# Kernel tuning notes

Hardware: AMD Instinct MI355X
Metric: run time of the kernel (lower is better)

The kernel has to match this reference:

```python
import jax, jax.numpy as jnp
import numpy as np

E, H = 512, 256  # embed_dim, hidden_dim
B, SQ, SK = 2, 512, 512


def _linear_params(k, fin, fout):
    lim = 1.0 / np.sqrt(fin)
    kw, kb = jax.random.split(k)
    W = jax.random.uniform(kw, (fin, fout), minval=-lim, maxval=lim, dtype=jnp.float32)
    b = jax.random.uniform(kb, (fout,), minval=-lim, maxval=lim, dtype=jnp.float32)
    return W, b


def setup_inputs() -> dict:
    rng = jax.random.key(0)
    ks = jax.random.split(rng, 12)
    query = jax.random.normal(ks[0], (B, SQ, E), dtype=jnp.float32)
    key = jax.random.normal(ks[1], (B, SK, E), dtype=jnp.float32)
    Wqe, bqe = _linear_params(ks[2], E, H)
    Wke, bke = _linear_params(ks[3], E, H)
    W1, b1 = _linear_params(ks[4], 2 * H, H)  # importance_predictor layer 0
    W2, b2 = _linear_params(ks[5], H, H)      # layer 1
    W3, b3 = _linear_params(ks[6], H, H)      # layer 2
    Wf, bf = _linear_params(ks[7], H, 1)      # final importance logit
    Wv1, bv1 = _linear_params(ks[8], 2 * H, H)  # variance_estimator layer 0
    Wv2, bv2 = _linear_params(ks[9], H, 1)      # variance_estimator final
    return {"query": query, "key": key,
            "Wqe": Wqe, "bqe": bqe, "Wke": Wke, "bke": bke,
            "W1": W1, "b1": b1, "W2": W2, "b2": b2, "W3": W3, "b3": b3,
            "Wf": Wf, "bf": bf, "Wv1": Wv1, "bv1": bv1, "Wv2": Wv2, "bv2": bv2}


def reference(query, key, Wqe, bqe, Wke, bke, W1, b1, W2, b2, W3, b3, Wf, bf, Wv1, bv1, Wv2, bv2):
    # Encoders (dropout is identity at eval)
    qf = jax.nn.relu(jnp.einsum('bqe,eh->bqh', query, Wqe) + bqe)  # [B,Sq,H]
    kf = jax.nn.relu(jnp.einsum('bke,eh->bkh', key, Wke) + bke)    # [B,Sk,H]

    # First Linear(2H,H) on cat([q,k]) == q@W1[:H] + k@W1[H:]; broadcast over pairs
    qp = jnp.einsum('bqh,hd->bqd', qf, W1[:H])
    kp = jnp.einsum('bkh,hd->bkd', kf, W1[H:])
    h = jax.nn.relu(qp[:, :, None, :] + kp[:, None, :, :] + b1)  # [B,Sq,Sk,H]
    h = jax.nn.relu(jnp.einsum('bqkh,hd->bqkd', h, W2) + b2)
    h = jax.nn.relu(jnp.einsum('bqkh,hd->bqkd', h, W3) + b3)
    importance_logits = (jnp.einsum('bqkh,ho->bqko', h, Wf) + bf)[..., 0]  # [B,Sq,Sk]

    # Variance head: Linear(2H,H) split the same way, ReLU, Linear, Softplus
    vq = jnp.einsum('bqh,hd->bqd', qf, Wv1[:H])
    vk = jnp.einsum('bkh,hd->bkd', kf, Wv1[H:])
    v = jax.nn.relu(vq[:, :, None, :] + vk[:, None, :, :] + bv1)  # [B,Sq,Sk,H]
    estimated_variance = jax.nn.softplus((jnp.einsum('bqkh,ho->bqko', v, Wv2) + bv2)[..., 0])
    return importance_logits, estimated_variance
```

## Files before the change

kernel.cpp:

```cpp
#include <hip/hip_runtime.h>
#include <hip/hip_bf16.h>
#include <cstdint>
#include <cstddef>
#include <cstring>

#define HDIM 256
#define EDIM 512
#define NB   2
#define NSQ  512
#define NSK  512

typedef _Float16 f16x8 __attribute__((ext_vector_type(8)));
typedef _Float16 h2    __attribute__((ext_vector_type(2)));
typedef __fp16   fp16v2 __attribute__((ext_vector_type(2)));
typedef float    f32x4  __attribute__((ext_vector_type(4)));

#define OFF_W2F  0u
#define OFF_W3F  65536u
#define OFF_WQEF 131072u
#define OFF_WKEF 262144u
#define OFF_WCQ  393216u
#define OFF_WCK  524288u
#define OFF_WV2H 655360u
#define F16_WS_END_BYTES 1312768u

union U8 { f16x8 v; h2 h[4]; };

__device__ __forceinline__ ushort2 f2h2(float x, float y) {
  fp16v2 r = __builtin_amdgcn_cvt_pkrtz(x, y);
  ushort2 u;
  __builtin_memcpy(&u, &r, 4);
  return u;
}
__device__ __forceinline__ float relu_(float x) { return x > 0.f ? x : 0.f; }
__device__ __forceinline__ float softplus_(float x) {
  return fmaxf(x, 0.f) + log1pf(expf(-fabsf(x)));
}

__global__ __launch_bounds__(256) void shuffle_weights(
    const float* __restrict__ Wqe, const float* __restrict__ Wke,
    const float* __restrict__ W1,  const float* __restrict__ Wv1,
    const float* __restrict__ W2,  const float* __restrict__ W3,
    const float* __restrict__ Wv2,
    unsigned short* __restrict__ wsb)
{
  __shared__ float sW[32 * 257];
  const int bx = blockIdx.x;
  const int t = threadIdx.x;
  if (bx == 80) {
    if (t < 64) {
      float a = Wv2[t * 4 + 0], b = Wv2[t * 4 + 1];
      float c = Wv2[t * 4 + 2], d = Wv2[t * 4 + 3];
      ushort2 lo = f2h2(a, b), hi = f2h2(c, d);
      ushort4 o; o.x = lo.x; o.y = lo.y; o.z = hi.x; o.w = hi.y;
      *(ushort4*)&wsb[OFF_WV2H + t * 4] = o;
    }
    return;
  }
  const float* src; unsigned short* dst; int s; int S;
  if      (bx <  8) { src = W2;          dst = wsb + OFF_W2F;           s = bx;      S = 8;  }
  else if (bx < 16) { src = W3;          dst = wsb + OFF_W3F;           s = bx - 8;  S = 8;  }
  else if (bx < 32) { src = Wqe;         dst = wsb + OFF_WQEF;          s = bx - 16; S = 16; }
  else if (bx < 48) { src = Wke;         dst = wsb + OFF_WKEF;          s = bx - 32; S = 16; }
  else if (bx < 56) { src = W1;          dst = wsb + OFF_WCQ;           s = bx - 48; S = 8;  }
  else if (bx < 64) { src = Wv1;         dst = wsb + OFF_WCQ + 65536u;  s = bx - 56; S = 8;  }
  else if (bx < 72) { src = W1 + 65536;  dst = wsb + OFF_WCK;           s = bx - 64; S = 8;  }
  else              { src = Wv1 + 65536; dst = wsb + OFF_WCK + 65536u;  s = bx - 72; S = 8;  }

  const int kbase = s * 32;
  #pragma unroll
  for (int it = 0; it < 8; ++it) {
    const int f4 = it * 256 + t;
    const int row = f4 >> 6, c4 = (f4 & 63) * 4;
    float4 v = *(const float4*)(src + (size_t)(kbase + row) * 256 + c4);
    sW[row * 257 + c4 + 0] = v.x; sW[row * 257 + c4 + 1] = v.y;
    sW[row * 257 + c4 + 2] = v.z; sW[row * 257 + c4 + 3] = v.w;
  }
  __syncthreads();

  const int wave = t >> 6, lane = t & 63;
  const int n_in = lane & 15, k0 = (lane >> 4) * 8;
  for (int tt = wave * 4; tt < wave * 4 + 4; ++tt) {
    const int n = tt * 16 + n_in;
    float x[8];
    #pragma unroll
    for (int j = 0; j < 8; ++j) x[j] = sW[(k0 + j) * 257 + n];
    ushort2 p0 = f2h2(x[0], x[1]), p1 = f2h2(x[2], x[3]);
    ushort2 p2 = f2h2(x[4], x[5]), p3 = f2h2(x[6], x[7]);
    ushort4 lo; lo.x = p0.x; lo.y = p0.y; lo.z = p1.x; lo.w = p1.y;
    ushort4 hi; hi.x = p2.x; hi.y = p2.y; hi.z = p3.x; hi.w = p3.y;
    unsigned short* o = dst + ((size_t)(tt * S + s) * 64 + lane) * 8;
    *(ushort4*)&o[0] = lo; *(ushort4*)&o[4] = hi;
  }
}

__global__ __launch_bounds__(512) void encoder_kernel(
    const float* __restrict__ query, const float* __restrict__ key,
    const float* __restrict__ bqe,   const float* __restrict__ bke,
    const float* __restrict__ b1,    const float* __restrict__ bv1,
    const unsigned short* __restrict__ WqeF, const unsigned short* __restrict__ WkeF,
    const unsigned short* __restrict__ WcqF, const unsigned short* __restrict__ WckF,
    _Float16* __restrict__ Pq, _Float16* __restrict__ Pk)
{
  __shared__ unsigned short sX[16 * 520];
  __shared__ unsigned short sF[16 * 264];
  __shared__ float sBe[256];
  __shared__ float sBc[512];

  const int bx   = blockIdx.x;
  const int side = bx >> 8;
  const int idx  = bx & 255;
  const int rt   = idx >> 2;
  const int nh   = idx & 3;
  const int t    = threadIdx.x;

  const float* Xsrc = side ? key : query;
  const unsigned short* WeF = side ? WkeF : WqeF;
  const unsigned short* WcF = side ? WckF : WcqF;
  _Float16* P = side ? Pk : Pq;

  const int wave = t >> 6, lane = t & 63;
  const int l15 = lane & 15, q4 = lane >> 4;

  const unsigned short* aeb = WeF + ((size_t)(wave * 2) * 16 * 64 + lane) * 8;
  f16x8 afe[2][2];
  #pragma unroll
  for (int ft = 0; ft < 2; ++ft)
    afe[0][ft] = *(const f16x8*)(aeb + ft * 8192);

  {
    const int m = t >> 5, ch = t & 31;
    const float* xr = Xsrc + (size_t)(rt * 16 + m) * EDIM;
    #pragma unroll
    for (int j = 0; j < 4; ++j) {
      const int c = j * 128 + ch * 4;
      float4 v = *(const float4*)(xr + c);
      ushort2 lo = f2h2(v.x, v.y), hi = f2h2(v.z, v.w);
      ushort4 xb; xb.x = lo.x; xb.y = lo.y; xb.z = hi.x; xb.w = hi.y;
      *(ushort4*)&sX[m * 520 + c] = xb;
    }
    if (t < 256) {
      sBe[t]       = side ? bke[t] : bqe[t];
      sBc[t]       = side ? 0.f : b1[t];
      sBc[256 + t] = side ? 0.f : bv1[t];
    }
  }
  __syncthreads();

  f32x4 acc1[2];
  #pragma unroll
  for (int ft = 0; ft < 2; ++ft) acc1[ft] = (f32x4){0.f, 0.f, 0.f, 0.f};

  #pragma unroll
  for (int s = 0; s < 16; ++s) {
    if (s < 15) {
      #pragma unroll
      for (int ft = 0; ft < 2; ++ft)
        afe[(s + 1) & 1][ft] = *(const f16x8*)(aeb + ft * 8192 + (size_t)(s + 1) * 512);
    }
    f16x8 bfr = *(const f16x8*)&sX[l15 * 520 + s * 32 + q4 * 8];
    #pragma unroll
    for (int ft = 0; ft < 2; ++ft)
      acc1[ft] = __builtin_amdgcn_mfma_f32_16x16x32_f16(afe[s & 1][ft], bfr, acc1[ft], 0, 0, 0);
  }

  #pragma unroll
  for (int ft = 0; ft < 2; ++ft) {
    const int tg = wave * 2 + ft;
    const int n0 = tg * 16 + q4 * 4;
    float4 b4 = *(const float4*)&sBe[n0];
    f32x4 a = acc1[ft];
    ushort2 lo = f2h2(relu_(a[0] + b4.x), relu_(a[1] + b4.y));
    ushort2 hi = f2h2(relu_(a[2] + b4.z), relu_(a[3] + b4.w));
    ushort4 h; h.x = lo.x; h.y = lo.y; h.z = hi.x; h.w = hi.y;
    *(ushort4*)&sF[l15 * 264 + n0] = h;
  }
  __syncthreads();

  const int tg2 = nh * 8 + wave;
  const unsigned short* acb = WcF + ((size_t)tg2 * 8 * 64 + lane) * 8;
  f16x8 afc[2];
  afc[0] = *(const f16x8*)(acb);

  f32x4 acc2 = (f32x4){0.f, 0.f, 0.f, 0.f};

  #pragma unroll
  for (int s = 0; s < 8; ++s) {
    if (s < 7)
      afc[(s + 1) & 1] = *(const f16x8*)(acb + (size_t)(s + 1) * 512);
    f16x8 bfr = *(const f16x8*)&sF[l15 * 264 + s * 32 + q4 * 8];
    acc2 = __builtin_amdgcn_mfma_f32_16x16x32_f16(afc[s & 1], bfr, acc2, 0, 0, 0);
  }

  {
    const int n0 = tg2 * 16 + q4 * 4;
    float4 bc = *(const float4*)&sBc[n0];
    const int row = rt * 16 + l15;
    ushort2 lo = f2h2(acc2[0] + bc.x, acc2[1] + bc.y);
    ushort2 hi = f2h2(acc2[2] + bc.z, acc2[3] + bc.w);
    ushort4 o; o.x = lo.x; o.y = lo.y; o.z = hi.x; o.w = hi.y;
    *(ushort4*)((unsigned short*)P + (size_t)row * 512 + n0) = o;
  }
}

__global__ __launch_bounds__(512, 4) void pair_kernel(
    const _Float16* __restrict__ Pq, const _Float16* __restrict__ Pk,
    const unsigned short* __restrict__ W2F, const unsigned short* __restrict__ W3F,
    const float* __restrict__ b2, const float* __restrict__ b3,
    const float* __restrict__ Wf, const float* __restrict__ bfp,
    const unsigned short* __restrict__ Wv2H, const float* __restrict__ bv2p,
    float* __restrict__ out)
{
  __shared__ __align__(16) unsigned char smem[69632];
  unsigned short* sXH = (unsigned short*)smem;
  unsigned short* sH  = (unsigned short*)(smem + 33792);
  float* sRed = (float*)(smem + 67584);

  const int kt = blockIdx.x, qy = blockIdx.y, bz = blockIdx.z;
  const int t = threadIdx.x;
  const _Float16* qpRow = Pq + (size_t)(bz * NSQ + qy) * 512;

  const int wave = t >> 6, lane = t & 63;
  const int l15 = lane & 15, q4 = lane >> 4;

  const unsigned short* a2base = W2F + ((size_t)(wave * 2) * 8 * 64 + lane) * 8;
  const unsigned short* a3base = W3F + ((size_t)(wave * 2) * 8 * 64 + lane) * 8;

  f16x8 afd[2][2];
  afd[0][0] = *(const f16x8*)(a2base);
  afd[0][1] = *(const f16x8*)(a2base + 8 * 64 * 8);

  float vp0 = 0.f, vp1 = 0.f;
  {
    const int m   = t >> 3;
    const int sub = t & 7;
    const _Float16* kpRow = Pk + (size_t)(bz * NSK + kt * 64 + m) * 512;
    const f16x8 z8 = {0, 0, 0, 0, 0, 0, 0, 0};
    #pragma unroll
    for (int it = 0; it < 4; ++it) {
      const int c = it * 64 + sub * 8;
      f16x8 q8 = *(const f16x8*)(qpRow + c);
      f16x8 k8 = *(const f16x8*)(kpRow + c);
      f16x8 r  = __builtin_elementwise_max(q8 + k8, z8);
      *(f16x8*)&sXH[m * 264 + c] = r;
      f16x8 a8 = *(const f16x8*)(qpRow + 256 + c);
      f16x8 v8 = *(const f16x8*)(kpRow + 256 + c);
      U8 ar; ar.v = __builtin_elementwise_max(a8 + v8, z8);
      U8 w8; w8.v = *(const f16x8*)((const _Float16*)Wv2H + c);
      vp0 = __builtin_amdgcn_fdot2(ar.h[0], w8.h[0], vp0, false);
      vp1 = __builtin_amdgcn_fdot2(ar.h[1], w8.h[1], vp1, false);
      vp0 = __builtin_amdgcn_fdot2(ar.h[2], w8.h[2], vp0, false);
      vp1 = __builtin_amdgcn_fdot2(ar.h[3], w8.h[3], vp1, false);
    }
  }
  __syncthreads();

  f32x4 acc[2][4];
  #pragma unroll
  for (int ft = 0; ft < 2; ++ft)
    #pragma unroll
    for (int pt = 0; pt < 4; ++pt)
      acc[ft][pt] = (f32x4){0.f, 0.f, 0.f, 0.f};

  f16x8 bcur[4], bnxt[4];
  #pragma unroll
  for (int pt = 0; pt < 4; ++pt)
    bcur[pt] = *(const f16x8*)&sXH[(pt * 16 + l15) * 264 + q4 * 8];

  #pragma unroll
  for (int s = 0; s < 8; ++s) {
    if (s < 7) {
      afd[(s + 1) & 1][0] = *(const f16x8*)(a2base + (size_t)(s + 1) * 512);
      afd[(s + 1) & 1][1] = *(const f16x8*)(a2base + 8 * 64 * 8 + (size_t)(s + 1) * 512);
      #pragma unroll
      for (int pt = 0; pt < 4; ++pt)
        bnxt[pt] = *(const f16x8*)&sXH[(pt * 16 + l15) * 264 + (s + 1) * 32 + q4 * 8];
    }
    __builtin_amdgcn_s_setprio(1);
    #pragma unroll
    for (int ft = 0; ft < 2; ++ft)
      #pragma unroll
      for (int pt = 0; pt < 4; ++pt)
        acc[ft][pt] = __builtin_amdgcn_mfma_f32_16x16x32_f16(afd[s & 1][ft], bcur[pt], acc[ft][pt], 0, 0, 0);
    __builtin_amdgcn_s_setprio(0);
    #pragma unroll
    for (int pt = 0; pt < 4; ++pt) bcur[pt] = bnxt[pt];
  }

  afd[0][0] = *(const f16x8*)(a3base);
  afd[0][1] = *(const f16x8*)(a3base + 8 * 64 * 8);

  #pragma unroll
  for (int ft = 0; ft < 2; ++ft) {
    const int tg = wave * 2 + ft;
    const int n0 = tg * 16 + q4 * 4;
    float4 b4 = *(const float4*)&b2[n0];
    #pragma unroll
    for (int pt = 0; pt < 4; ++pt) {
      const int mr = pt * 16 + l15;
      f32x4 a = acc[ft][pt];
      ushort2 lo = f2h2(relu_(a[0] + b4.x), relu_(a[1] + b4.y));
      ushort2 hi = f2h2(relu_(a[2] + b4.z), relu_(a[3] + b4.w));
      ushort4 h; h.x = lo.x; h.y = lo.y; h.z = hi.x; h.w = hi.y;
      *(ushort4*)&sH[mr * 264 + n0] = h;
    }
  }
  __syncthreads();

  f32x4 acc2[2][4];
  #pragma unroll
  for (int ft = 0; ft < 2; ++ft)
    #pragma unroll
    for (int pt = 0; pt < 4; ++pt)
      acc2[ft][pt] = (f32x4){0.f, 0.f, 0.f, 0.f};

  #pragma unroll
  for (int pt = 0; pt < 4; ++pt)
    bcur[pt] = *(const f16x8*)&sH[(pt * 16 + l15) * 264 + q4 * 8];

  #pragma unroll
  for (int s = 0; s < 8; ++s) {
    if (s < 7) {
      afd[(s + 1) & 1][0] = *(const f16x8*)(a3base + (size_t)(s + 1) * 512);
      afd[(s + 1) & 1][1] = *(const f16x8*)(a3base + 8 * 64 * 8 + (size_t)(s + 1) * 512);
      #pragma unroll
      for (int pt = 0; pt < 4; ++pt)
        bnxt[pt] = *(const f16x8*)&sH[(pt * 16 + l15) * 264 + (s + 1) * 32 + q4 * 8];
    }
    __builtin_amdgcn_s_setprio(1);
    #pragma unroll
    for (int ft = 0; ft < 2; ++ft)
      #pragma unroll
      for (int pt = 0; pt < 4; ++pt)
        acc2[ft][pt] = __builtin_amdgcn_mfma_f32_16x16x32_f16(afd[s & 1][ft], bcur[pt], acc2[ft][pt], 0, 0, 0);
    __builtin_amdgcn_s_setprio(0);
    #pragma unroll
    for (int pt = 0; pt < 4; ++pt) bcur[pt] = bnxt[pt];
  }

  {
    float v = vp0 + vp1;
    v += __shfl_xor(v, 1, 64);
    v += __shfl_xor(v, 2, 64);
    v += __shfl_xor(v, 4, 64);
    if ((t & 7) == 0) {
      const int m = t >> 3;
      const size_t o = (size_t)(bz * NSQ + qy) * NSK + kt * 64 + m;
      out[(size_t)NB * NSQ * NSK + o] = softplus_(v + bv2p[0]);
    }
  }

  float p[4] = {0.f, 0.f, 0.f, 0.f};
  #pragma unroll
  for (int ft = 0; ft < 2; ++ft) {
    const int tg = wave * 2 + ft;
    const int n0 = tg * 16 + q4 * 4;
    float4 b4 = *(const float4*)&b3[n0];
    float4 w4 = *(const float4*)&Wf[n0];
    #pragma unroll
    for (int pt = 0; pt < 4; ++pt) {
      f32x4 a = acc2[ft][pt];
      p[pt] += relu_(a[0] + b4.x) * w4.x + relu_(a[1] + b4.y) * w4.y
             + relu_(a[2] + b4.z) * w4.z + relu_(a[3] + b4.w) * w4.w;
    }
  }
  #pragma unroll
  for (int pt = 0; pt < 4; ++pt) {
    float v = p[pt];
    v += __shfl_xor(v, 16, 64);
    v += __shfl_xor(v, 32, 64);
    if (lane < 16) sRed[wave * 64 + pt * 16 + lane] = v;
  }
  __syncthreads();

  if (t < 64) {
    const size_t o = (size_t)(bz * NSQ + qy) * NSK + kt * 64 + t;
    float lg = bfp[0];
    #pragma unroll
    for (int w = 0; w < 8; ++w) lg += sRed[w * 64 + t];
    out[o] = lg;
  }
}

extern "C" void kernel_launch(void* const* d_in, const int* in_sizes, int n_in,
                              void* d_out, int out_size, void* d_ws, size_t ws_size,
                              hipStream_t stream)
{
  (void)in_sizes; (void)n_in; (void)out_size; (void)ws_size;
  const float* query = (const float*)d_in[0];
  const float* key   = (const float*)d_in[1];
  const float* Wqe   = (const float*)d_in[2];
  const float* bqe   = (const float*)d_in[3];
  const float* Wke   = (const float*)d_in[4];
  const float* bke   = (const float*)d_in[5];
  const float* W1    = (const float*)d_in[6];
  const float* b1    = (const float*)d_in[7];
  const float* W2    = (const float*)d_in[8];
  const float* b2    = (const float*)d_in[9];
  const float* W3    = (const float*)d_in[10];
  const float* b3    = (const float*)d_in[11];
  const float* Wf    = (const float*)d_in[12];
  const float* bf    = (const float*)d_in[13];
  const float* Wv1   = (const float*)d_in[14];
  const float* bv1   = (const float*)d_in[15];
  const float* Wv2   = (const float*)d_in[16];
  const float* bv2   = (const float*)d_in[17];

  unsigned short* wsb = (unsigned short*)d_ws;
  _Float16* Pq = (_Float16*)((char*)d_ws + F16_WS_END_BYTES);
  _Float16* Pk = Pq + (size_t)1024 * 512;
  float* out = (float*)d_out;

  shuffle_weights<<<81, 256, 0, stream>>>(Wqe, Wke, W1, Wv1, W2, W3, Wv2, wsb);
  encoder_kernel<<<512, 512, 0, stream>>>(query, key, bqe, bke, b1, bv1,
      wsb + OFF_WQEF, wsb + OFF_WKEF, wsb + OFF_WCQ, wsb + OFF_WCK, Pq, Pk);
  pair_kernel<<<dim3(NSK / 64, NSQ, NB), 512, 0, stream>>>(Pq, Pk,
      wsb + OFF_W2F, wsb + OFF_W3F, b2, b3, Wf, bf, wsb + OFF_WV2H, bv2, out);
}
```

Measured before the change: 255.1 us.

## Make pair kernel persistent over key tiles with async LDS staging of key projections

Each block now handles one query row and loops over all eight 64-key tiles, instead of launching one block per (key tile, query) pair. Raw key projections are staged into LDS with global_load_lds, and the next tile is prefetched while the second GEMM runs. The q+k add and ReLU are fused into the MFMA operand load. This cuts the block count and the per-block setup and repeated loads, but gives eight times fewer blocks and adds a serial loop with extra barriers per tile.

```diff
diff --git a/kernel.cpp b/kernel.cpp
--- a/kernel.cpp
+++ b/kernel.cpp
@@ -211,175 +211,227 @@
     const unsigned short* __restrict__ Wv2H, const float* __restrict__ bv2p,
     float* __restrict__ out)
 {
-  __shared__ __align__(16) unsigned char smem[69632];
-  unsigned short* sXH = (unsigned short*)smem;
+  __shared__ __align__(16) unsigned char smem[70656];
+  unsigned short* sKP = (unsigned short*)smem;
   unsigned short* sH  = (unsigned short*)(smem + 33792);
-  float* sRed = (float*)(smem + 67584);
-
-  const int kt = blockIdx.x, qy = blockIdx.y, bz = blockIdx.z;
+  unsigned short* sQP = (unsigned short*)(smem + 67584);
+  float* sRed = (float*)(smem + 68608);
+
+  const int qy = blockIdx.x, bz = blockIdx.y;
   const int t = threadIdx.x;
-  const _Float16* qpRow = Pq + (size_t)(bz * NSQ + qy) * 512;
 
   const int wave = t >> 6, lane = t & 63;
   const int l15 = lane & 15, q4 = lane >> 4;
+  const int m8 = t >> 3, sub = t & 7;
+
+  const _Float16* qpRow = Pq + (size_t)(bz * NSQ + qy) * 512;
+  const _Float16* PkB   = Pk + (size_t)(bz * NSK) * 512;
 
   const unsigned short* a2base = W2F + ((size_t)(wave * 2) * 8 * 64 + lane) * 8;
   const unsigned short* a3base = W3F + ((size_t)(wave * 2) * 8 * 64 + lane) * 8;
 
+  const f16x8 z8 = {0, 0, 0, 0, 0, 0, 0, 0};
+
+  #define STAGE_KP(ktile)                                                      \
+    do {                                                                       \
+      const _Float16* kb_ = PkB + (size_t)(ktile) * 64 * 512;                  \
+      _Pragma("unroll")                                                        \
+      for (int i_ = 0; i_ < 4; ++i_) {                                         \
+        const int chunk_ = i_ * 512 + t;                                       \
+        const int r_ = chunk_ / 33;                                            \
+        const int c_ = chunk_ - r_ * 33;                                       \
+        const int cc_ = (c_ == 32) ? 0 : c_;                                   \
+        const _Float16* g_ = kb_ + (size_t)r_ * 512 + cc_ * 8;                 \
+        unsigned short* l_ = sKP + (size_t)(i_ * 512 + (t & ~63)) * 8;         \
+        __builtin_amdgcn_global_load_lds(                                      \
+            (const __attribute__((address_space(1))) unsigned int*)g_,         \
+            (__attribute__((address_space(3))) unsigned int*)l_, 16, 0, 0);    \
+      }                                                                        \
+      if (t < 64) {                                                            \
+        const int chunk_ = 2048 + t;                                           \
+        const int r_ = chunk_ / 33;                                            \
+        const int c_ = chunk_ - r_ * 33;                                       \
+        const int cc_ = (c_ == 32) ? 0 : c_;                                   \
+        const _Float16* g_ = kb_ + (size_t)r_ * 512 + cc_ * 8;                 \
+        unsigned short* l_ = sKP + (size_t)2048 * 8;                           \
+        __builtin_amdgcn_global_load_lds(                                      \
+            (const __attribute__((address_space(1))) unsigned int*)g_,         \
+            (__attribute__((address_space(3))) unsigned int*)l_, 16, 0, 0);    \
+      }                                                                        \
+    } while (0)
+
+  if (t < 64) *(f16x8*)&sQP[t * 8] = *(const f16x8*)(qpRow + t * 8);
+  STAGE_KP(0);
   f16x8 afd[2][2];
   afd[0][0] = *(const f16x8*)(a2base);
-  afd[0][1] = *(const f16x8*)(a2base + 8 * 64 * 8);
-
-  float vp0 = 0.f, vp1 = 0.f;
-  {
-    const int m   = t >> 3;
-    const int sub = t & 7;
-    const _Float16* kpRow = Pk + (size_t)(bz * NSK + kt * 64 + m) * 512;
-    const f16x8 z8 = {0, 0, 0, 0, 0, 0, 0, 0};
-    #pragma unroll
-    for (int it = 0; it < 4; ++it) {
-      const int c = it * 64 + sub * 8;
-      f16x8 q8 = *(const f16x8*)(qpRow + c);
-      f16x8 k8 = *(const f16x8*)(kpRow + c);
-      f16x8 r  = __builtin_elementwise_max(q8 + k8, z8);
-      *(f16x8*)&sXH[m * 264 + c] = r;
-      f16x8 a8 = *(const f16x8*)(qpRow + 256 + c);
-      f16x8 v8 = *(const f16x8*)(kpRow + 256 + c);
-      U8 ar; ar.v = __builtin_elementwise_max(a8 + v8, z8);
-      U8 w8; w8.v = *(const f16x8*)((const _Float16*)Wv2H + c);
-      vp0 = __builtin_amdgcn_fdot2(ar.h[0], w8.h[0], vp0, false);
-      vp1 = __builtin_amdgcn_fdot2(ar.h[1], w8.h[1], vp1, false);
-      vp0 = __builtin_amdgcn_fdot2(ar.h[2], w8.h[2], vp0, false);
-      vp1 = __builtin_amdgcn_fdot2(ar.h[3], w8.h[3], vp1, false);
-    }
-  }
+  afd[0][1] = *(const f16x8*)(a2base + 4096);
   __syncthreads();
 
-  f32x4 acc[2][4];
-  #pragma unroll
-  for (int ft = 0; ft < 2; ++ft)
+  for (int kt = 0; kt < 8; ++kt) {
+    f32x4 acc[2][4];
+    #pragma unroll
+    for (int ft = 0; ft < 2; ++ft)
+      #pragma unroll
+      for (int pt = 0; pt < 4; ++pt)
+        acc[ft][pt] = (f32x4){0.f, 0.f, 0.f, 0.f};
+
+    f16x8 bcur[4], brnx[4];
+    {
+      f16x8 qpf = *(const f16x8*)&sQP[q4 * 8];
+      #pragma unroll
+      for (int pt = 0; pt < 4; ++pt) {
+        f16x8 raw = *(const f16x8*)&sKP[(pt * 16 + l15) * 264 + q4 * 8];
+        bcur[pt] = __builtin_elementwise_max(raw + qpf, z8);
+      }
+    }
+
+    #pragma unroll
+    for (int s = 0; s < 8; ++s) {
+      f16x8 qpn;
+      if (s < 7) {
+        afd[(s + 1) & 1][0] = *(const f16x8*)(a2base + (size_t)(s + 1) * 512);
+        afd[(s + 1) & 1][1] = *(const f16x8*)(a2base + 4096 + (size_t)(s + 1) * 512);
+        qpn = *(const f16x8*)&sQP[(s + 1) * 32 + q4 * 8];
+        #pragma unroll
+        for (int pt = 0; pt < 4; ++pt)
+          brnx[pt] = *(const f16x8*)&sKP[(pt * 16 + l15) * 264 + (s + 1) * 32 + q4 * 8];
+      }
+      __builtin_amdgcn_s_setprio(1);
+      #pragma unroll
+      for (int ft = 0; ft < 2; ++ft)
+        #pragma unroll
+        for (int pt = 0; pt < 4; ++pt)
+          acc[ft][pt] = __builtin_amdgcn_mfma_f32_16x16x32_f16(afd[s & 1][ft], bcur[pt], acc[ft][pt], 0, 0, 0);
+      __builtin_amdgcn_s_setprio(0);
+      if (s < 7) {
+        #pragma unroll
+        for (int pt = 0; pt < 4; ++pt)
+          bcur[pt] = __builtin_elementwise_max(brnx[pt] + qpn, z8);
+      }
+    }
+
+    afd[0][0] = *(const f16x8*)(a3base);
+    afd[0][1] = *(const f16x8*)(a3base + 4096);
+
+    #pragma unroll
+    for (int ft = 0; ft < 2; ++ft) {
+      const int tg = wave * 2 + ft;
+      const int n0 = tg * 16 + q4 * 4;
+      float4 b4 = *(const float4*)&b2[n0];
+      #pragma unroll
+      for (int pt = 0; pt < 4; ++pt) {
+        const int mr = pt * 16 + l15;
+        f32x4 a = acc[ft][pt];
+        ushort2 lo = f2h2(relu_(a[0] + b4.x), relu_(a[1] + b4.y));
+        ushort2 hi = f2h2(relu_(a[2] + b4.z), relu_(a[3] + b4.w));
+        ushort4 h; h.x = lo.x; h.y = lo.y; h.z = hi.x; h.w = hi.y;
+        *(ushort4*)&sH[mr * 264 + n0] = h;
+      }
+    }
+    __syncthreads();
+
+    if (kt < 7) STAGE_KP(kt + 1);
+
+    f16x8 kv[4];
+    {
+      const _Float16* kvRow = PkB + ((size_t)(kt * 64 + m8)) * 512 + 256;
+      #pragma unroll
+      for (int it = 0; it < 4; ++it)
+        kv[it] = *(const f16x8*)(kvRow + it * 64 + sub * 8);
+    }
+
+    #pragma unroll
+    for (int ft = 0; ft < 2; ++ft)
+      #pragma unroll
+      for (int pt = 0; pt < 4; ++pt)
+        acc[ft][pt] = (f32x4){0.f, 0.f, 0.f, 0.f};
+
     #pragma unroll
     for (int pt = 0; pt < 4; ++pt)
-      acc[ft][pt] = (f32x4){0.f, 0.f, 0.f, 0.f};
-
-  f16x8 bcur[4], bnxt[4];
-  #pragma unroll
-  for (int pt = 0; pt < 4; ++pt)
-    bcur[pt] = *(const f16x8*)&sXH[(pt * 16 + l15) * 264 + q4 * 8];
-
-  #pragma unroll
-  for (int s = 0; s < 8; ++s) {
-    if (s < 7) {
-      afd[(s + 1) & 1][0] = *(const f16x8*)(a2base + (size_t)(s + 1) * 512);
-      afd[(s + 1) & 1][1] = *(const f16x8*)(a2base + 8 * 64 * 8 + (size_t)(s + 1) * 512);
-      #pragma unroll
-      for (int pt = 0; pt < 4; ++pt)
-        bnxt[pt] = *(const f16x8*)&sXH[(pt * 16 + l15) * 264 + (s + 1) * 32 + q4 * 8];
-    }
-    __builtin_amdgcn_s_setprio(1);
-    #pragma unroll
-    for (int ft = 0; ft < 2; ++ft)
-      #pragma unroll
-      for (int pt = 0; pt < 4; ++pt)
-        acc[ft][pt] = __builtin_amdgcn_mfma_f32_16x16x32_f16(afd[s & 1][ft], bcur[pt], acc[ft][pt], 0, 0, 0);
-    __builtin_amdgcn_s_setprio(0);
-    #pragma unroll
-    for (int pt = 0; pt < 4; ++pt) bcur[pt] = bnxt[pt];
-  }
-
-  afd[0][0] = *(const f16x8*)(a3base);
-  afd[0][1] = *(const f16x8*)(a3base + 8 * 64 * 8);
-
-  #pragma unroll
-  for (int ft = 0; ft < 2; ++ft) {
-    const int tg = wave * 2 + ft;
-    const int n0 = tg * 16 + q4 * 4;
-    float4 b4 = *(const float4*)&b2[n0];
-    #pragma unroll
-    for (int pt = 0; pt < 4; ++pt) {
-      const int mr = pt * 16 + l15;
-      f32x4 a = acc[ft][pt];
-      ushort2 lo = f2h2(relu_(a[0] + b4.x), relu_(a[1] + b4.y));
-      ushort2 hi = f2h2(relu_(a[2] + b4.z), relu_(a[3] + b4.w));
-      ushort4 h; h.x = lo.x; h.y = lo.y; h.z = hi.x; h.w = hi.y;
-      *(ushort4*)&sH[mr * 264 + n0] = h;
-    }
-  }
-  __syncthreads();
-
-  f32x4 acc2[2][4];
-  #pragma unroll
-  for (int ft = 0; ft < 2; ++ft)
-    #pragma unroll
-    for (int pt = 0; pt < 4; ++pt)
-      acc2[ft][pt] = (f32x4){0.f, 0.f, 0.f, 0.f};
-
-  #pragma unroll
-  for (int pt = 0; pt < 4; ++pt)
-    bcur[pt] = *(const f16x8*)&sH[(pt * 16 + l15) * 264 + q4 * 8];
-
-  #pragma unroll
-  for (int s = 0; s < 8; ++s) {
-    if (s < 7) {
-      afd[(s + 1) & 1][0] = *(const f16x8*)(a3base + (size_t)(s + 1) * 512);
-      afd[(s + 1) & 1][1] = *(const f16x8*)(a3base + 8 * 64 * 8 + (size_t)(s + 1) * 512);
-      #pragma unroll
-      for (int pt = 0; pt < 4; ++pt)
-        bnxt[pt] = *(const f16x8*)&sH[(pt * 16 + l15) * 264 + (s + 1) * 32 + q4 * 8];
-    }
-    __builtin_amdgcn_s_setprio(1);
-    #pragma unroll
-    for (int ft = 0; ft < 2; ++ft)
-      #pragma unroll
-      for (int pt = 0; pt < 4; ++pt)
-        acc2[ft][pt] = __builtin_amdgcn_mfma_f32_16x16x32_f16(afd[s & 1][ft], bcur[pt], acc2[ft][pt], 0, 0, 0);
-    __builtin_amdgcn_s_setprio(0);
-    #pragma unroll
-    for (int pt = 0; pt < 4; ++pt) bcur[pt] = bnxt[pt];
-  }
-
-  {
-    float v = vp0 + vp1;
-    v += __shfl_xor(v, 1, 64);
-    v += __shfl_xor(v, 2, 64);
-    v += __shfl_xor(v, 4, 64);
-    if ((t & 7) == 0) {
-      const int m = t >> 3;
-      const size_t o = (size_t)(bz * NSQ + qy) * NSK + kt * 64 + m;
-      out[(size_t)NB * NSQ * NSK + o] = softplus_(v + bv2p[0]);
-    }
-  }
-
-  float p[4] = {0.f, 0.f, 0.f, 0.f};
-  #pragma unroll
-  for (int ft = 0; ft < 2; ++ft) {
-    const int tg = wave * 2 + ft;
-    const int n0 = tg * 16 + q4 * 4;
-    float4 b4 = *(const float4*)&b3[n0];
-    float4 w4 = *(const float4*)&Wf[n0];
-    #pragma unroll
-    for (int pt = 0; pt < 4; ++pt) {
-      f32x4 a = acc2[ft][pt];
-      p[pt] += relu_(a[0] + b4.x) * w4.x + relu_(a[1] + b4.y) * w4.y
-             + relu_(a[2] + b4.z) * w4.z + relu_(a[3] + b4.w) * w4.w;
-    }
-  }
-  #pragma unroll
-  for (int pt = 0; pt < 4; ++pt) {
-    float v = p[pt];
-    v += __shfl_xor(v, 16, 64);
-    v += __shfl_xor(v, 32, 64);
-    if (lane < 16) sRed[wave * 64 + pt * 16 + lane] = v;
-  }
-  __syncthreads();
-
-  if (t < 64) {
-    const size_t o = (size_t)(bz * NSQ + qy) * NSK + kt * 64 + t;
-    float lg = bfp[0];
-    #pragma unroll
-    for (int w = 0; w < 8; ++w) lg += sRed[w * 64 + t];
-    out[o] = lg;
-  }
+      bcur[pt] = *(const f16x8*)&sH[(pt * 16 + l15) * 264 + q4 * 8];
+
+    #pragma unroll
+    for (int s = 0; s < 8; ++s) {
+      if (s < 7) {
+        afd[(s + 1) & 1][0] = *(const f16x8*)(a3base + (size_t)(s + 1) * 512);
+        afd[(s + 1) & 1][1] = *(const f16x8*)(a3base + 4096 + (size_t)(s + 1) * 512);
+        #pragma unroll
+        for (int pt = 0; pt < 4; ++pt)
+          brnx[pt] = *(const f16x8*)&sH[(pt * 16 + l15) * 264 + (s + 1) * 32 + q4 * 8];
+      }
+      __builtin_amdgcn_s_setprio(1);
+      #pragma unroll
+      for (int ft = 0; ft < 2; ++ft)
+        #pragma unroll
+        for (int pt = 0; pt < 4; ++pt)
+          acc[ft][pt] = __builtin_amdgcn_mfma_f32_16x16x32_f16(afd[s & 1][ft], bcur[pt], acc[ft][pt], 0, 0, 0);
+      __builtin_amdgcn_s_setprio(0);
+      if (s < 7) {
+        #pragma unroll
+        for (int pt = 0; pt < 4; ++pt) bcur[pt] = brnx[pt];
+      }
+    }
+
+    afd[0][0] = *(const f16x8*)(a2base);
+    afd[0][1] = *(const f16x8*)(a2base + 4096);
+
+    {
+      float vp0 = 0.f, vp1 = 0.f;
+      #pragma unroll
+      for (int it = 0; it < 4; ++it) {
+        const int c = it * 64 + sub * 8;
+        f16x8 qv8 = *(const f16x8*)&sQP[256 + c];
+        U8 ar; ar.v = __builtin_elementwise_max(kv[it] + qv8, z8);
+        U8 w8; w8.v = *(const f16x8*)((const _Float16*)Wv2H + c);
+        vp0 = __builtin_amdgcn_fdot2(ar.h[0], w8.h[0], vp0, false);
+        vp1 = __builtin_amdgcn_fdot2(ar.h[1], w8.h[1], vp1, false);
+        vp0 = __builtin_amdgcn_fdot2(ar.h[2], w8.h[2], vp0, false);
+        vp1 = __builtin_amdgcn_fdot2(ar.h[3], w8.h[3], vp1, false);
+      }
+      float v = vp0 + vp1;
+      v += __shfl_xor(v, 1, 64);
+      v += __shfl_xor(v, 2, 64);
+      v += __shfl_xor(v, 4, 64);
+      if (sub == 0) {
+        const size_t o = (size_t)(bz * NSQ + qy) * NSK + kt * 64 + m8;
+        out[(size_t)NB * NSQ * NSK + o] = softplus_(v + bv2p[0]);
+      }
+    }
+
+    {
+      float p[4] = {0.f, 0.f, 0.f, 0.f};
+      #pragma unroll
+      for (int ft = 0; ft < 2; ++ft) {
+        const int tg = wave * 2 + ft;
+        const int n0 = tg * 16 + q4 * 4;
+        float4 b4 = *(const float4*)&b3[n0];
+        float4 w4 = *(const float4*)&Wf[n0];
+        #pragma unroll
+        for (int pt = 0; pt < 4; ++pt) {
+          f32x4 a = acc[ft][pt];
+          p[pt] += relu_(a[0] + b4.x) * w4.x + relu_(a[1] + b4.y) * w4.y
+                 + relu_(a[2] + b4.z) * w4.z + relu_(a[3] + b4.w) * w4.w;
+        }
+      }
+      #pragma unroll
+      for (int pt = 0; pt < 4; ++pt) {
+        float v = p[pt];
+        v += __shfl_xor(v, 16, 64);
+        v += __shfl_xor(v, 32, 64);
+        if (lane < 16) sRed[wave * 64 + pt * 16 + lane] = v;
+      }
+    }
+    __syncthreads();
+
+    if (t < 64) {
+      const size_t o = (size_t)(bz * NSQ + qy) * NSK + kt * 64 + t;
+      float lg = bfp[0];
+      #pragma unroll
+      for (int w = 0; w < 8; ++w) lg += sRed[w * 64 + t];
+      out[o] = lg;
+    }
+  }
+  #undef STAGE_KP
 }
 
 extern "C" void kernel_launch(void* const* d_in, const int* in_sizes, int n_in,
@@ -414,6 +466,6 @@
   shuffle_weights<<<81, 256, 0, stream>>>(Wqe, Wke, W1, Wv1, W2, W3, Wv2, wsb);
   encoder_kernel<<<512, 512, 0, stream>>>(query, key, bqe, bke, b1, bv1,
       wsb + OFF_WQEF, wsb + OFF_WKEF, wsb + OFF_WCQ, wsb + OFF_WCK, Pq, Pk);
-  pair_kernel<<<dim3(NSK / 64, NSQ, NB), 512, 0, stream>>>(Pq, Pk,
+  pair_kernel<<<dim3(NSQ, NB), 512, 0, stream>>>(Pq, Pk,
       wsb + OFF_W2F, wsb + OFF_W3F, b2, b3, Wf, bf, wsb + OFF_WV2H, bv2, out);
 }
```

Result: slower. 537.0 us (+110.5%).

## Use 1024-thread pair blocks with one feature tile per wave and reuse LDS

Applied to the files above, without the earlier changes.

The pair kernel now runs 16 waves per block instead of 8. Each wave computes one 16-column feature tile instead of two, which halves per-wave accumulator registers. The second-layer hidden activations overwrite the input tile in shared memory, so shared memory per block roughly halves; this needs an extra barrier. Register double-buffering of the A and B fragments and the setprio hints are dropped, trading software prefetch for more resident waves to hide latency, and the final cross-wave reduction grows to 16 partials.

```diff
diff --git a/kernel.cpp b/kernel.cpp
--- a/kernel.cpp
+++ b/kernel.cpp
@@ -203,7 +203,7 @@
   }
 }
 
-__global__ __launch_bounds__(512, 4) void pair_kernel(
+__global__ __launch_bounds__(1024, 8) void pair_kernel(
     const _Float16* __restrict__ Pq, const _Float16* __restrict__ Pk,
     const unsigned short* __restrict__ W2F, const unsigned short* __restrict__ W3F,
     const float* __restrict__ b2, const float* __restrict__ b3,
@@ -211,34 +211,27 @@
     const unsigned short* __restrict__ Wv2H, const float* __restrict__ bv2p,
     float* __restrict__ out)
 {
-  __shared__ __align__(16) unsigned char smem[69632];
+  __shared__ __align__(16) unsigned char smem[37888];
   unsigned short* sXH = (unsigned short*)smem;
-  unsigned short* sH  = (unsigned short*)(smem + 33792);
-  float* sRed = (float*)(smem + 67584);
+  float* sRed = (float*)(smem + 33792);
 
   const int kt = blockIdx.x, qy = blockIdx.y, bz = blockIdx.z;
   const int t = threadIdx.x;
-  const _Float16* qpRow = Pq + (size_t)(bz * NSQ + qy) * 512;
 
   const int wave = t >> 6, lane = t & 63;
   const int l15 = lane & 15, q4 = lane >> 4;
 
-  const unsigned short* a2base = W2F + ((size_t)(wave * 2) * 8 * 64 + lane) * 8;
-  const unsigned short* a3base = W3F + ((size_t)(wave * 2) * 8 * 64 + lane) * 8;
-
-  f16x8 afd[2][2];
-  afd[0][0] = *(const f16x8*)(a2base);
-  afd[0][1] = *(const f16x8*)(a2base + 8 * 64 * 8);
+  const _Float16* qpRow = Pq + (size_t)(bz * NSQ + qy) * 512;
 
   float vp0 = 0.f, vp1 = 0.f;
   {
-    const int m   = t >> 3;
-    const int sub = t & 7;
+    const int m = t >> 4;
+    const int sub = t & 15;
     const _Float16* kpRow = Pk + (size_t)(bz * NSK + kt * 64 + m) * 512;
     const f16x8 z8 = {0, 0, 0, 0, 0, 0, 0, 0};
     #pragma unroll
-    for (int it = 0; it < 4; ++it) {
-      const int c = it * 64 + sub * 8;
+    for (int it = 0; it < 2; ++it) {
+      const int c = it * 128 + sub * 8;
       f16x8 q8 = *(const f16x8*)(qpRow + c);
       f16x8 k8 = *(const f16x8*)(kpRow + c);
       f16x8 r  = __builtin_elementwise_max(q8 + k8, z8);
@@ -255,87 +248,50 @@
   }
   __syncthreads();
 
-  f32x4 acc[2][4];
-  #pragma unroll
-  for (int ft = 0; ft < 2; ++ft)
-    #pragma unroll
-    for (int pt = 0; pt < 4; ++pt)
-      acc[ft][pt] = (f32x4){0.f, 0.f, 0.f, 0.f};
-
-  f16x8 bcur[4], bnxt[4];
-  #pragma unroll
-  for (int pt = 0; pt < 4; ++pt)
-    bcur[pt] = *(const f16x8*)&sXH[(pt * 16 + l15) * 264 + q4 * 8];
+  const unsigned short* a2 = W2F + (size_t)wave * 4096 + lane * 8;
+  const unsigned short* a3 = W3F + (size_t)wave * 4096 + lane * 8;
+  const int n0 = wave * 16 + q4 * 4;
+
+  f32x4 acc[4];
+  #pragma unroll
+  for (int pt = 0; pt < 4; ++pt) acc[pt] = (f32x4){0.f, 0.f, 0.f, 0.f};
 
   #pragma unroll
   for (int s = 0; s < 8; ++s) {
-    if (s < 7) {
-      afd[(s + 1) & 1][0] = *(const f16x8*)(a2base + (size_t)(s + 1) * 512);
-      afd[(s + 1) & 1][1] = *(const f16x8*)(a2base + 8 * 64 * 8 + (size_t)(s + 1) * 512);
-      #pragma unroll
-      for (int pt = 0; pt < 4; ++pt)
-        bnxt[pt] = *(const f16x8*)&sXH[(pt * 16 + l15) * 264 + (s + 1) * 32 + q4 * 8];
-    }
-    __builtin_amdgcn_s_setprio(1);
-    #pragma unroll
-    for (int ft = 0; ft < 2; ++ft)
-      #pragma unroll
-      for (int pt = 0; pt < 4; ++pt)
-        acc[ft][pt] = __builtin_amdgcn_mfma_f32_16x16x32_f16(afd[s & 1][ft], bcur[pt], acc[ft][pt], 0, 0, 0);
-    __builtin_amdgcn_s_setprio(0);
-    #pragma unroll
-    for (int pt = 0; pt < 4; ++pt) bcur[pt] = bnxt[pt];
-  }
-
-  afd[0][0] = *(const f16x8*)(a3base);
-  afd[0][1] = *(const f16x8*)(a3base + 8 * 64 * 8);
-
-  #pragma unroll
-  for (int ft = 0; ft < 2; ++ft) {
-    const int tg = wave * 2 + ft;
-    const int n0 = tg * 16 + q4 * 4;
+    f16x8 af = *(const f16x8*)(a2 + (size_t)s * 512);
+    #pragma unroll
+    for (int pt = 0; pt < 4; ++pt) {
+      f16x8 bf = *(const f16x8*)&sXH[(pt * 16 + l15) * 264 + s * 32 + q4 * 8];
+      acc[pt] = __builtin_amdgcn_mfma_f32_16x16x32_f16(af, bf, acc[pt], 0, 0, 0);
+    }
+  }
+  __syncthreads();
+
+  {
     float4 b4 = *(const float4*)&b2[n0];
     #pragma unroll
     for (int pt = 0; pt < 4; ++pt) {
       const int mr = pt * 16 + l15;
-      f32x4 a = acc[ft][pt];
+      f32x4 a = acc[pt];
       ushort2 lo = f2h2(relu_(a[0] + b4.x), relu_(a[1] + b4.y));
       ushort2 hi = f2h2(relu_(a[2] + b4.z), relu_(a[3] + b4.w));
       ushort4 h; h.x = lo.x; h.y = lo.y; h.z = hi.x; h.w = hi.y;
-      *(ushort4*)&sH[mr * 264 + n0] = h;
-    }
-  }
-  __syncthreads();
-
-  f32x4 acc2[2][4];
-  #pragma unroll
-  for (int ft = 0; ft < 2; ++ft)
-    #pragma unroll
-    for (int pt = 0; pt < 4; ++pt)
-      acc2[ft][pt] = (f32x4){0.f, 0.f, 0.f, 0.f};
-
-  #pragma unroll
-  for (int pt = 0; pt < 4; ++pt)
-    bcur[pt] = *(const f16x8*)&sH[(pt * 16 + l15) * 264 + q4 * 8];
+      *(ushort4*)&sXH[mr * 264 + n0] = h;
+    }
+  }
+  __syncthreads();
+
+  #pragma unroll
+  for (int pt = 0; pt < 4; ++pt) acc[pt] = (f32x4){0.f, 0.f, 0.f, 0.f};
 
   #pragma unroll
   for (int s = 0; s < 8; ++s) {
-    if (s < 7) {
-      afd[(s + 1) & 1][0] = *(const f16x8*)(a3base + (size_t)(s + 1) * 512);
-      afd[(s + 1) & 1][1] = *(const f16x8*)(a3base + 8 * 64 * 8 + (size_t)(s + 1) * 512);
-      #pragma unroll
-      for (int pt = 0; pt < 4; ++pt)
-        bnxt[pt] = *(const f16x8*)&sH[(pt * 16 + l15) * 264 + (s + 1) * 32 + q4 * 8];
-    }
-    __builtin_amdgcn_s_setprio(1);
-    #pragma unroll
-    for (int ft = 0; ft < 2; ++ft)
-      #pragma unroll
-      for (int pt = 0; pt < 4; ++pt)
-        acc2[ft][pt] = __builtin_amdgcn_mfma_f32_16x16x32_f16(afd[s & 1][ft], bcur[pt], acc2[ft][pt], 0, 0, 0);
-    __builtin_amdgcn_s_setprio(0);
-    #pragma unroll
-    for (int pt = 0; pt < 4; ++pt) bcur[pt] = bnxt[pt];
+    f16x8 af = *(const f16x8*)(a3 + (size_t)s * 512);
+    #pragma unroll
+    for (int pt = 0; pt < 4; ++pt) {
+      f16x8 bf = *(const f16x8*)&sXH[(pt * 16 + l15) * 264 + s * 32 + q4 * 8];
+      acc[pt] = __builtin_amdgcn_mfma_f32_16x16x32_f16(af, bf, acc[pt], 0, 0, 0);
+    }
   }
 
   {
@@ -343,33 +299,31 @@
     v += __shfl_xor(v, 1, 64);
     v += __shfl_xor(v, 2, 64);
     v += __shfl_xor(v, 4, 64);
-    if ((t & 7) == 0) {
-      const int m = t >> 3;
+    v += __shfl_xor(v, 8, 64);
+    if (l15 == 0) {
+      const int m = wave * 4 + q4;
       const size_t o = (size_t)(bz * NSQ + qy) * NSK + kt * 64 + m;
       out[(size_t)NB * NSQ * NSK + o] = softplus_(v + bv2p[0]);
     }
   }
 
-  float p[4] = {0.f, 0.f, 0.f, 0.f};
-  #pragma unroll
-  for (int ft = 0; ft < 2; ++ft) {
-    const int tg = wave * 2 + ft;
-    const int n0 = tg * 16 + q4 * 4;
+  {
+    float p[4] = {0.f, 0.f, 0.f, 0.f};
     float4 b4 = *(const float4*)&b3[n0];
     float4 w4 = *(const float4*)&Wf[n0];
     #pragma unroll
     for (int pt = 0; pt < 4; ++pt) {
-      f32x4 a = acc2[ft][pt];
+      f32x4 a = acc[pt];
       p[pt] += relu_(a[0] + b4.x) * w4.x + relu_(a[1] + b4.y) * w4.y
              + relu_(a[2] + b4.z) * w4.z + relu_(a[3] + b4.w) * w4.w;
     }
-  }
-  #pragma unroll
-  for (int pt = 0; pt < 4; ++pt) {
-    float v = p[pt];
-    v += __shfl_xor(v, 16, 64);
-    v += __shfl_xor(v, 32, 64);
-    if (lane < 16) sRed[wave * 64 + pt * 16 + lane] = v;
+    #pragma unroll
+    for (int pt = 0; pt < 4; ++pt) {
+      float v = p[pt];
+      v += __shfl_xor(v, 16, 64);
+      v += __shfl_xor(v, 32, 64);
+      if (lane < 16) sRed[wave * 64 + pt * 16 + lane] = v;
+    }
   }
   __syncthreads();
 
@@ -377,7 +331,7 @@
     const size_t o = (size_t)(bz * NSQ + qy) * NSK + kt * 64 + t;
     float lg = bfp[0];
     #pragma unroll
-    for (int w = 0; w < 8; ++w) lg += sRed[w * 64 + t];
+    for (int w = 0; w < 16; ++w) lg += sRed[w * 64 + t];
     out[o] = lg;
   }
 }
@@ -414,6 +368,6 @@
   shuffle_weights<<<81, 256, 0, stream>>>(Wqe, Wke, W1, Wv1, W2, W3, Wv2, wsb);
   encoder_kernel<<<512, 512, 0, stream>>>(query, key, bqe, bke, b1, bv1,
       wsb + OFF_WQEF, wsb + OFF_WKEF, wsb + OFF_WCQ, wsb + OFF_WCK, Pq, Pk);
-  pair_kernel<<<dim3(NSK / 64, NSQ, NB), 512, 0, stream>>>(Pq, Pk,
+  pair_kernel<<<dim3(NSK / 64, NSQ, NB), 1024, 0, stream>>>(Pq, Pk,
       wsb + OFF_W2F, wsb + OFF_W3F, b2, b3, Wf, bf, wsb + OFF_WV2H, bv2, out);
 }
```

Result: slower. 291.3 us (+14.2%).

## Retile pair-kernel MFMA work as 2x4 wave grid and drop register prefetch

Applied to the files above, without the earlier changes.

Each of the eight waves now owns a 32-row by 64-column output tile (2 M-groups by 4 N-groups) instead of 64 rows by 32 columns. Each wave therefore loads four global weight fragments and two LDS activation fragments per k-step, where before it loaded two and four. The cross-iteration double-buffered prefetch of A and B fragments is removed and fragments are loaded inside each step, which cuts register pressure. The reduction buffer shrinks to four partial rows. The trade-off is more global weight traffic per wave and less explicit latency hiding.

```diff
diff --git a/kernel.cpp b/kernel.cpp
--- a/kernel.cpp
+++ b/kernel.cpp
@@ -211,7 +211,7 @@
     const unsigned short* __restrict__ Wv2H, const float* __restrict__ bv2p,
     float* __restrict__ out)
 {
-  __shared__ __align__(16) unsigned char smem[69632];
+  __shared__ __align__(16) unsigned char smem[68608];
   unsigned short* sXH = (unsigned short*)smem;
   unsigned short* sH  = (unsigned short*)(smem + 33792);
   float* sRed = (float*)(smem + 67584);
@@ -222,13 +222,11 @@
 
   const int wave = t >> 6, lane = t & 63;
   const int l15 = lane & 15, q4 = lane >> 4;
-
-  const unsigned short* a2base = W2F + ((size_t)(wave * 2) * 8 * 64 + lane) * 8;
-  const unsigned short* a3base = W3F + ((size_t)(wave * 2) * 8 * 64 + lane) * 8;
-
-  f16x8 afd[2][2];
-  afd[0][0] = *(const f16x8*)(a2base);
-  afd[0][1] = *(const f16x8*)(a2base + 8 * 64 * 8);
+  const int mi = wave >> 2;
+  const int ni = wave & 3;
+
+  const unsigned short* a2base = W2F + ((size_t)(ni * 4) * 8 * 64 + lane) * 8;
+  const unsigned short* a3base = W3F + ((size_t)(ni * 4) * 8 * 64 + lane) * 8;
 
   float vp0 = 0.f, vp1 = 0.f;
   {
@@ -255,49 +253,39 @@
   }
   __syncthreads();
 
-  f32x4 acc[2][4];
-  #pragma unroll
-  for (int ft = 0; ft < 2; ++ft)
-    #pragma unroll
-    for (int pt = 0; pt < 4; ++pt)
+  f32x4 acc[4][2];
+  #pragma unroll
+  for (int ft = 0; ft < 4; ++ft)
+    #pragma unroll
+    for (int pt = 0; pt < 2; ++pt)
       acc[ft][pt] = (f32x4){0.f, 0.f, 0.f, 0.f};
 
-  f16x8 bcur[4], bnxt[4];
-  #pragma unroll
-  for (int pt = 0; pt < 4; ++pt)
-    bcur[pt] = *(const f16x8*)&sXH[(pt * 16 + l15) * 264 + q4 * 8];
-
   #pragma unroll
   for (int s = 0; s < 8; ++s) {
-    if (s < 7) {
-      afd[(s + 1) & 1][0] = *(const f16x8*)(a2base + (size_t)(s + 1) * 512);
-      afd[(s + 1) & 1][1] = *(const f16x8*)(a2base + 8 * 64 * 8 + (size_t)(s + 1) * 512);
+    f16x8 afd[4], bf[2];
+    #pragma unroll
+    for (int ft = 0; ft < 4; ++ft)
+      afd[ft] = *(const f16x8*)(a2base + ft * 4096 + (size_t)s * 512);
+    #pragma unroll
+    for (int pt = 0; pt < 2; ++pt)
+      bf[pt] = *(const f16x8*)&sXH[(mi * 32 + pt * 16 + l15) * 264 + s * 32 + q4 * 8];
+    __builtin_amdgcn_s_setprio(1);
+    #pragma unroll
+    for (int ft = 0; ft < 4; ++ft)
       #pragma unroll
-      for (int pt = 0; pt < 4; ++pt)
-        bnxt[pt] = *(const f16x8*)&sXH[(pt * 16 + l15) * 264 + (s + 1) * 32 + q4 * 8];
-    }
-    __builtin_amdgcn_s_setprio(1);
-    #pragma unroll
-    for (int ft = 0; ft < 2; ++ft)
-      #pragma unroll
-      for (int pt = 0; pt < 4; ++pt)
-        acc[ft][pt] = __builtin_amdgcn_mfma_f32_16x16x32_f16(afd[s & 1][ft], bcur[pt], acc[ft][pt], 0, 0, 0);
+      for (int pt = 0; pt < 2; ++pt)
+        acc[ft][pt] = __builtin_amdgcn_mfma_f32_16x16x32_f16(afd[ft], bf[pt], acc[ft][pt], 0, 0, 0);
     __builtin_amdgcn_s_setprio(0);
-    #pragma unroll
-    for (int pt = 0; pt < 4; ++pt) bcur[pt] = bnxt[pt];
-  }
-
-  afd[0][0] = *(const f16x8*)(a3base);
-  afd[0][1] = *(const f16x8*)(a3base + 8 * 64 * 8);
-
-  #pragma unroll
-  for (int ft = 0; ft < 2; ++ft) {
-    const int tg = wave * 2 + ft;
+  }
+
+  #pragma unroll
+  for (int ft = 0; ft < 4; ++ft) {
+    const int tg = ni * 4 + ft;
     const int n0 = tg * 16 + q4 * 4;
     float4 b4 = *(const float4*)&b2[n0];
     #pragma unroll
-    for (int pt = 0; pt < 4; ++pt) {
-      const int mr = pt * 16 + l15;
+    for (int pt = 0; pt < 2; ++pt) {
+      const int mr = mi * 32 + pt * 16 + l15;
       f32x4 a = acc[ft][pt];
       ushort2 lo = f2h2(relu_(a[0] + b4.x), relu_(a[1] + b4.y));
       ushort2 hi = f2h2(relu_(a[2] + b4.z), relu_(a[3] + b4.w));
@@ -307,35 +295,28 @@
   }
   __syncthreads();
 
-  f32x4 acc2[2][4];
-  #pragma unroll
-  for (int ft = 0; ft < 2; ++ft)
-    #pragma unroll
-    for (int pt = 0; pt < 4; ++pt)
-      acc2[ft][pt] = (f32x4){0.f, 0.f, 0.f, 0.f};
-
-  #pragma unroll
-  for (int pt = 0; pt < 4; ++pt)
-    bcur[pt] = *(const f16x8*)&sH[(pt * 16 + l15) * 264 + q4 * 8];
+  #pragma unroll
+  for (int ft = 0; ft < 4; ++ft)
+    #pragma unroll
+    for (int pt = 0; pt < 2; ++pt)
+      acc[ft][pt] = (f32x4){0.f, 0.f, 0.f, 0.f};
 
   #pragma unroll
   for (int s = 0; s < 8; ++s) {
-    if (s < 7) {
-      afd[(s + 1) & 1][0] = *(const f16x8*)(a3base + (size_t)(s + 1) * 512);
-      afd[(s + 1) & 1][1] = *(const f16x8*)(a3base + 8 * 64 * 8 + (size_t)(s + 1) * 512);
+    f16x8 afd[4], bf[2];
+    #pragma unroll
+    for (int ft = 0; ft < 4; ++ft)
+      afd[ft] = *(const f16x8*)(a3base + ft * 4096 + (size_t)s * 512);
+    #pragma unroll
+    for (int pt = 0; pt < 2; ++pt)
+      bf[pt] = *(const f16x8*)&sH[(mi * 32 + pt * 16 + l15) * 264 + s * 32 + q4 * 8];
+    __builtin_amdgcn_s_setprio(1);
+    #pragma unroll
+    for (int ft = 0; ft < 4; ++ft)
       #pragma unroll
-      for (int pt = 0; pt < 4; ++pt)
-        bnxt[pt] = *(const f16x8*)&sH[(pt * 16 + l15) * 264 + (s + 1) * 32 + q4 * 8];
-    }
-    __builtin_amdgcn_s_setprio(1);
-    #pragma unroll
-    for (int ft = 0; ft < 2; ++ft)
-      #pragma unroll
-      for (int pt = 0; pt < 4; ++pt)
-        acc2[ft][pt] = __builtin_amdgcn_mfma_f32_16x16x32_f16(afd[s & 1][ft], bcur[pt], acc2[ft][pt], 0, 0, 0);
+      for (int pt = 0; pt < 2; ++pt)
+        acc[ft][pt] = __builtin_amdgcn_mfma_f32_16x16x32_f16(afd[ft], bf[pt], acc[ft][pt], 0, 0, 0);
     __builtin_amdgcn_s_setprio(0);
-    #pragma unroll
-    for (int pt = 0; pt < 4; ++pt) bcur[pt] = bnxt[pt];
   }
 
   {
@@ -350,26 +331,28 @@
     }
   }
 
-  float p[4] = {0.f, 0.f, 0.f, 0.f};
-  #pragma unroll
-  for (int ft = 0; ft < 2; ++ft) {
-    const int tg = wave * 2 + ft;
-    const int n0 = tg * 16 + q4 * 4;
-    float4 b4 = *(const float4*)&b3[n0];
-    float4 w4 = *(const float4*)&Wf[n0];
-    #pragma unroll
-    for (int pt = 0; pt < 4; ++pt) {
-      f32x4 a = acc2[ft][pt];
-      p[pt] += relu_(a[0] + b4.x) * w4.x + relu_(a[1] + b4.y) * w4.y
-             + relu_(a[2] + b4.z) * w4.z + relu_(a[3] + b4.w) * w4.w;
-    }
-  }
-  #pragma unroll
-  for (int pt = 0; pt < 4; ++pt) {
-    float v = p[pt];
-    v += __shfl_xor(v, 16, 64);
-    v += __shfl_xor(v, 32, 64);
-    if (lane < 16) sRed[wave * 64 + pt * 16 + lane] = v;
+  {
+    float p[2] = {0.f, 0.f};
+    #pragma unroll
+    for (int ft = 0; ft < 4; ++ft) {
+      const int tg = ni * 4 + ft;
+      const int n0 = tg * 16 + q4 * 4;
+      float4 b4 = *(const float4*)&b3[n0];
+      float4 w4 = *(const float4*)&Wf[n0];
+      #pragma unroll
+      for (int pt = 0; pt < 2; ++pt) {
+        f32x4 a = acc[ft][pt];
+        p[pt] += relu_(a[0] + b4.x) * w4.x + relu_(a[1] + b4.y) * w4.y
+               + relu_(a[2] + b4.z) * w4.z + relu_(a[3] + b4.w) * w4.w;
+      }
+    }
+    #pragma unroll
+    for (int pt = 0; pt < 2; ++pt) {
+      float v = p[pt];
+      v += __shfl_xor(v, 16, 64);
+      v += __shfl_xor(v, 32, 64);
+      if (lane < 16) sRed[ni * 64 + mi * 32 + pt * 16 + lane] = v;
+    }
   }
   __syncthreads();
 
@@ -377,7 +360,7 @@
     const size_t o = (size_t)(bz * NSQ + qy) * NSK + kt * 64 + t;
     float lg = bfp[0];
     #pragma unroll
-    for (int w = 0; w < 8; ++w) lg += sRed[w * 64 + t];
+    for (int w = 0; w < 4; ++w) lg += sRed[w * 64 + t];
     out[o] = lg;
   }
 }
```

Result: slower. 290.2 us (+13.8%).
